# Performance work log

Hardware: AMD Instinct MI355X
Metric: run time of the kernel (lower is better)

Reference implementation:

```python
import jax, jax.numpy as jnp
import numpy as np

B, T, D, H = 4, 2048, 2048, 16
DH = D // H

def setup_inputs() -> dict:
    key = jax.random.key(0)
    ks = jax.random.split(key, 9)
    s = 1.0 / np.sqrt(D)
    return {
        "x": jax.random.normal(ks[0], (B, T, D), dtype=jnp.float32),
        "Wq": jax.random.uniform(ks[1], (D, D), jnp.float32, -s, s),
        "bq": jax.random.uniform(ks[2], (D,), jnp.float32, -s, s),
        "Wk": jax.random.uniform(ks[3], (D, D), jnp.float32, -s, s),
        "bk": jax.random.uniform(ks[4], (D,), jnp.float32, -s, s),
        "Wv": jax.random.uniform(ks[5], (D, D), jnp.float32, -s, s),
        "bv": jax.random.uniform(ks[6], (D,), jnp.float32, -s, s),
        "Wo": jax.random.uniform(ks[7], (D, D), jnp.float32, -s, s),
        "bo": jax.random.uniform(ks[8], (D,), jnp.float32, -s, s),
    }

def reference(x, Wq, bq, Wk, bk, Wv, bv, Wo, bo):
    # projections: [B,T,D] -> [B,H,T,DH]
    def split_heads(y):
        return y.reshape(B, T, H, DH).transpose(0, 2, 1, 3)
    q = split_heads(x @ Wq + bq)
    k = split_heads(x @ Wk + bk)
    v = split_heads(x @ Wv + bv)
    scale = DH ** -0.5
    scores = jnp.einsum('bhtd,bhsd->bhts', q, k) * scale  # [B,H,T,T]
    causal = jnp.tril(jnp.ones((T, T), dtype=bool))
    scores = jnp.where(causal[None, None], scores, -jnp.inf)
    weights = jax.nn.softmax(scores, axis=-1)
    out = jnp.einsum('bhts,bhsd->bhtd', weights, v)  # [B,H,T,DH]
    out = out.transpose(0, 2, 1, 3).reshape(B, T, D)
    return out @ Wo + bo
```

## Files before the change

kernel.cpp:

```cpp
#include <hip/hip_runtime.h>
#include <hip/hip_bf16.h>

#define B_  4
#define T_  2048
#define D_  2048
#define H_  16
#define DH_ 128

typedef __attribute__((ext_vector_type(4))) float f32x4;
typedef __attribute__((ext_vector_type(8))) short short8;
typedef __attribute__((ext_vector_type(4))) _Float16 half4;

__device__ __forceinline__ ushort f2bf(float f) {
    unsigned int u = __builtin_bit_cast(unsigned int, f);
    u += 0x7fffu + ((u >> 16) & 1u);
    return (ushort)(u >> 16);
}
__device__ __forceinline__ ushort f2h(float f) {
    return (ushort)(__builtin_bit_cast(unsigned int, __builtin_amdgcn_cvt_pkrtz(f, f)) & 0xffffu);
}

__device__ __forceinline__ void glds16(const void* g, void* l) {
    __builtin_amdgcn_global_load_lds(
        (const __attribute__((address_space(1))) unsigned int*)g,
        (__attribute__((address_space(3))) unsigned int*)l, 16, 0, 0);
}

__global__ void cast_f32_bf16(const float* __restrict__ x, ushort* __restrict__ xb, int n) {
    int i = (blockIdx.x * 256 + threadIdx.x) * 4;
    if (i < n) {
        float4 v = *(const float4*)(x + i);
        ushort4 o;
        o.x = f2bf(v.x); o.y = f2bf(v.y); o.z = f2bf(v.z); o.w = f2bf(v.w);
        *(ushort4*)(xb + i) = o;
    }
}

__global__ void transpose_cast4(
    const float* __restrict__ W0, const float* __restrict__ W1,
    const float* __restrict__ W2, const float* __restrict__ W3,
    ushort* __restrict__ T0, ushort* __restrict__ T1,
    ushort* __restrict__ T2, ushort* __restrict__ T3)
{
    const int z = blockIdx.z;
    const float* W = (z == 0) ? W0 : (z == 1) ? W1 : (z == 2) ? W2 : W3;
    ushort* Wt     = (z == 0) ? T0 : (z == 1) ? T1 : (z == 2) ? T2 : T3;
    __shared__ float tile[32][33];
    int tx = threadIdx.x, ty = threadIdx.y;
    int n0 = blockIdx.x * 32, k0 = blockIdx.y * 32;
#pragma unroll
    for (int i = 0; i < 4; i++)
        tile[ty + i * 8][tx] = W[(size_t)(k0 + ty + i * 8) * D_ + n0 + tx];
    __syncthreads();
#pragma unroll
    for (int i = 0; i < 4; i++)
        Wt[(size_t)(n0 + ty + i * 8) * D_ + k0 + tx] = f2bf(tile[tx][ty + i * 8]);
}

__global__ __launch_bounds__(256, 3) void gemm_qkv(
    const ushort* __restrict__ A,
    const ushort* __restrict__ Wq, const ushort* __restrict__ Wk, const ushort* __restrict__ Wv,
    const float* __restrict__ bq, const float* __restrict__ bk, const float* __restrict__ bv,
    ushort* __restrict__ Qb, ushort* __restrict__ Kb, ushort* __restrict__ Vtb,
    float qscale, int y0)
{
    extern __shared__ char smem[];
    uint4* sA = (uint4*)smem;
    uint4* sB = (uint4*)(smem + 8192);

    const int tid  = threadIdx.x;
    const int sel  = blockIdx.x >> 4;
    const int row0 = (blockIdx.y + y0) * 128, col0 = (blockIdx.x & 15) * 128;
    const ushort* Bt = (sel == 0) ? Wq : (sel == 1) ? Wk : Wv;
    const float* bias = (sel == 0) ? bq : (sel == 1) ? bk : bv;
    const float oscale = (sel == 0) ? qscale : 1.0f;
    const int K = D_, N = D_;

    const int mA = tid >> 2, g = tid & 3;
    const int gc = g ^ ((mA >> 2) & 3);
    const ushort* pa0 = A  + (size_t)(row0 + mA) * K + gc * 8;
    const ushort* pb0 = Bt + (size_t)(col0 + mA) * K + gc * 8;

    const int lane = tid & 63, w = tid >> 6;
    const int l15 = lane & 15, quad = lane >> 4;
    const int wm = w & 1, wn = w >> 1;
    const int csel = quad ^ ((l15 >> 2) & 3);
    int aoff[4], boff[4];
#pragma unroll
    for (int mt = 0; mt < 4; mt++) aoff[mt] = (wm * 64 + mt * 16 + l15) * 4 + csel;
#pragma unroll
    for (int nt = 0; nt < 4; nt++) boff[nt] = (wn * 64 + nt * 16 + l15) * 4 + csel;

    f32x4 acc[4][4] = {};

    const int kIter = K >> 5;
    for (int kt = 0; kt < kIter; ++kt) {
        if (kt) __syncthreads();
        glds16(pa0 + kt * 32,                     sA + tid);
        glds16(pa0 + kt * 32 + (size_t)64 * K,    sA + tid + 256);
        glds16(pb0 + kt * 32,                     sB + tid);
        glds16(pb0 + kt * 32 + (size_t)64 * K,    sB + tid + 256);
        __syncthreads();
        short8 af[4], bfr[4];
#pragma unroll
        for (int mt = 0; mt < 4; mt++) af[mt]  = __builtin_bit_cast(short8, sA[aoff[mt]]);
#pragma unroll
        for (int nt = 0; nt < 4; nt++) bfr[nt] = __builtin_bit_cast(short8, sB[boff[nt]]);
#pragma unroll
        for (int mt = 0; mt < 4; mt++)
#pragma unroll
            for (int nt = 0; nt < 4; nt++)
                acc[mt][nt] = __builtin_amdgcn_mfma_f32_16x16x32_bf16(af[mt], bfr[nt], acc[mt][nt], 0, 0, 0);
    }

    if (sel < 2) {
        ushort* Cout = (sel == 0) ? Qb : Kb;
#pragma unroll
        for (int nt = 0; nt < 4; nt++) {
            int col = col0 + wn * 64 + nt * 16 + l15;
            float bb = bias[col];
#pragma unroll
            for (int mt = 0; mt < 4; mt++) {
                int rowb = row0 + wm * 64 + mt * 16 + quad * 4;
#pragma unroll
                for (int r = 0; r < 4; ++r)
                    Cout[(size_t)(rowb + r) * N + col] = f2bf((acc[mt][nt][r] + bb) * oscale);
            }
        }
    } else {
        __syncthreads();
        ushort* tr = (ushort*)smem;
#pragma unroll
        for (int nt = 0; nt < 4; nt++) {
            int cl = wn * 64 + nt * 16 + l15;
            float bb = bias[col0 + cl];
#pragma unroll
            for (int mt = 0; mt < 4; mt++) {
                int rl = wm * 64 + mt * 16 + quad * 4;
#pragma unroll
                for (int r = 0; r < 4; ++r)
                    tr[cl * 136 + rl + r] = f2h(acc[mt][nt][r] + bb);
            }
        }
        __syncthreads();
        int b = row0 >> 11, t0 = row0 & (T_ - 1), h = col0 >> 7;
        for (int idx = tid; idx < 2048; idx += 256) {
            int dh = idx >> 4, c = idx & 15;
            uint4 v = *(const uint4*)(tr + dh * 136 + c * 8);
            *(uint4*)(Vtb + (size_t)((b * H_ + h) * DH_ + dh) * T_ + t0 + c * 8) = v;
        }
    }
}

__global__ __launch_bounds__(256, 4) void gemm_bt_f32(
    const ushort* __restrict__ A, const ushort* __restrict__ Bt,
    const float* __restrict__ bias, float* __restrict__ Cout,
    int M, int N, int K)
{
    extern __shared__ char smem[];
    uint4* sA = (uint4*)smem;
    uint4* sB = (uint4*)(smem + 8192);

    const int tid  = threadIdx.x;
    const int row0 = blockIdx.y * 128, col0 = blockIdx.x * 128;

    const int mA = tid >> 2, g = tid & 3;
    const int gc = g ^ ((mA >> 2) & 3);
    const ushort* pa0 = A  + (size_t)(row0 + mA) * K + gc * 8;
    const ushort* pb0 = Bt + (size_t)(col0 + mA) * K + gc * 8;

    const int lane = tid & 63, w = tid >> 6;
    const int l15 = lane & 15, quad = lane >> 4;
    const int wm = w & 1, wn = w >> 1;
    const int csel = quad ^ ((l15 >> 2) & 3);
    int aoff[4], boff[4];
#pragma unroll
    for (int mt = 0; mt < 4; mt++) aoff[mt] = (wm * 64 + mt * 16 + l15) * 4 + csel;
#pragma unroll
    for (int nt = 0; nt < 4; nt++) boff[nt] = (wn * 64 + nt * 16 + l15) * 4 + csel;

    f32x4 acc[4][4] = {};

    const int kIter = K >> 5;
    for (int kt = 0; kt < kIter; ++kt) {
        if (kt) __syncthreads();
        glds16(pa0 + kt * 32,                     sA + tid);
        glds16(pa0 + kt * 32 + (size_t)64 * K,    sA + tid + 256);
        glds16(pb0 + kt * 32,                     sB + tid);
        glds16(pb0 + kt * 32 + (size_t)64 * K,    sB + tid + 256);
        __syncthreads();
        short8 af[4], bfr[4];
#pragma unroll
        for (int mt = 0; mt < 4; mt++) af[mt]  = __builtin_bit_cast(short8, sA[aoff[mt]]);
#pragma unroll
        for (int nt = 0; nt < 4; nt++) bfr[nt] = __builtin_bit_cast(short8, sB[boff[nt]]);
#pragma unroll
        for (int mt = 0; mt < 4; mt++)
#pragma unroll
            for (int nt = 0; nt < 4; nt++)
                acc[mt][nt] = __builtin_amdgcn_mfma_f32_16x16x32_bf16(af[mt], bfr[nt], acc[mt][nt], 0, 0, 0);
    }

#pragma unroll
    for (int nt = 0; nt < 4; nt++) {
        int col = col0 + wn * 64 + nt * 16 + l15;
        float bb = bias[col];
#pragma unroll
        for (int mt = 0; mt < 4; mt++) {
            int rowb = row0 + wm * 64 + mt * 16 + quad * 4;
#pragma unroll
            for (int r = 0; r < 4; ++r)
                Cout[(size_t)(rowb + r) * N + col] = acc[mt][nt][r] + bb;
        }
    }
}

__global__ __launch_bounds__(256, 5) void attn_kernel(
    const ushort* __restrict__ Q, const ushort* __restrict__ K,
    const ushort* __restrict__ Vt, ushort* __restrict__ O)
{
    __shared__ __align__(16) char smem[32768];
    uint4*  kS = (uint4*)smem;
    ushort* vS = (ushort*)(smem + 16384);

    const int tid = threadIdx.x;
    const int bid = blockIdx.x;
    const int slot = bid >> 3;
    const int g = (bid & 7) + 8 * (slot >> 4);
    const int qx = slot & 15;
    const int b = g >> 4, h = g & 15;

    const int lane = tid & 63, w = tid >> 6, l15 = lane & 15, quad = lane >> 4;

    const int krow = tid >> 4;
    const int kchunk = (tid & 15) ^ (krow & 7);
    const ushort* kg = K + ((size_t)(b * T_) + krow) * D_ + h * DH_ + kchunk * 8;

    const int vrow = tid >> 3, vc = tid & 7;
    const ushort* vg = Vt + ((size_t)((b * H_ + h) * DH_) + vrow) * T_ + vc * 8;
    const int vs0 = ((2 * vc    ) ^ (vrow & 15)) * 4;
    const int vs1 = ((2 * vc + 1) ^ (vrow & 15)) * 4;

    const int qts[2] = { qx, 31 - qx };

    for (int e = 0; e < 2; ++e) {
        const int qt = qts[e], q0 = qt * 64;
        const int qbase = q0 + w * 16;

        short8 aq[4];
        {
            const ushort* qp = Q + ((size_t)(b * T_) + qbase + l15) * D_ + h * DH_ + quad * 8;
#pragma unroll
            for (int ks = 0; ks < 4; ++ks)
                aq[ks] = __builtin_bit_cast(short8, *(const uint4*)(qp + ks * 32));
        }

        f32x4 accO[8] = {};
        float mrow = -INFINITY, lrow = 0.f;

        auto tile = [&](int s0, int stMax, bool diag) {
            __syncthreads();
            const ushort* kp = kg + (size_t)s0 * D_;
#pragma unroll
            for (int j = 0; j < 4; ++j) glds16(kp + (size_t)j * 16 * D_, kS + j * 256 + tid);
            const ushort* vp = vg + s0;
            uint4 vv[4];
#pragma unroll
            for (int j = 0; j < 4; ++j) vv[j] = *(const uint4*)(vp + (size_t)j * 32 * T_);
#pragma unroll
            for (int j = 0; j < 4; ++j) {
                ushort* dst = vS + (j * 32 + vrow) * 64;
                *(uint2*)(dst + vs0) = make_uint2(vv[j].x, vv[j].y);
                *(uint2*)(dst + vs1) = make_uint2(vv[j].z, vv[j].w);
            }
            __syncthreads();

            f32x4 sT[4] = {};
#pragma unroll
            for (int ks = 0; ks < 4; ++ks)
#pragma unroll
                for (int st = 0; st < 4; ++st)
                    if (st < stMax) {
                        int row = st * 16 + l15;
                        short8 ak = __builtin_bit_cast(short8, kS[row * 16 + ((ks * 4 + quad) ^ (row & 7))]);
                        sT[st] = __builtin_amdgcn_mfma_f32_16x16x32_bf16(ak, aq[ks], sT[st], 0, 0, 0);
                    }

            if (diag) {
                const int q = qbase + l15;
                const int st = stMax - 1;
#pragma unroll
                for (int r = 0; r < 4; ++r)
                    if (s0 + st * 16 + quad * 4 + r > q) sT[st][r] = -INFINITY;
            }

            float rmax = -INFINITY;
#pragma unroll
            for (int st = 0; st < 4; ++st)
                if (st < stMax)
#pragma unroll
                    for (int r = 0; r < 4; ++r) rmax = fmaxf(rmax, sT[st][r]);
            rmax = fmaxf(rmax, __shfl_xor(rmax, 16));
            rmax = fmaxf(rmax, __shfl_xor(rmax, 32));
            float mnew  = fmaxf(mrow, rmax);
            float alpha = __builtin_amdgcn_exp2f(mrow - mnew);
            mrow = mnew;

            float psum = 0.f;
            half4 pb[4];
#pragma unroll
            for (int st = 0; st < 4; ++st)
                if (st < stMax) {
                    float p0 = __builtin_amdgcn_exp2f(sT[st][0] - mnew);
                    float p1 = __builtin_amdgcn_exp2f(sT[st][1] - mnew);
                    float p2 = __builtin_amdgcn_exp2f(sT[st][2] - mnew);
                    float p3 = __builtin_amdgcn_exp2f(sT[st][3] - mnew);
                    psum += (p0 + p1) + (p2 + p3);
                    uint2 u;
                    u.x = __builtin_bit_cast(unsigned int, __builtin_amdgcn_cvt_pkrtz(p0, p1));
                    u.y = __builtin_bit_cast(unsigned int, __builtin_amdgcn_cvt_pkrtz(p2, p3));
                    pb[st] = __builtin_bit_cast(half4, u);
                }
            psum += __shfl_xor(psum, 16);
            psum += __shfl_xor(psum, 32);
            lrow = lrow * alpha + psum;
#pragma unroll
            for (int nt = 0; nt < 8; ++nt)
#pragma unroll
                for (int r = 0; r < 4; ++r) accO[nt][r] *= alpha;

#pragma unroll
            for (int st = 0; st < 4; ++st)
                if (st < stMax) {
#pragma unroll
                    for (int nt = 0; nt < 8; ++nt) {
                        int dh = nt * 16 + l15;
                        half4 vf = *(const half4*)(vS + dh * 64 + (((st * 4 + quad) ^ l15) * 4));
                        accO[nt] = __builtin_amdgcn_mfma_f32_16x16x16f16(vf, pb[st], accO[nt], 0, 0, 0);
                    }
                }
        };

        for (int it = 0; it < qt; ++it) tile(it * 64, 4, false);
        tile(qt * 64, w + 1, true);

        __syncthreads();
        ushort* eT = (ushort*)smem + w * 2176;
        float inv = 1.0f / lrow;
#pragma unroll
        for (int nt = 0; nt < 8; ++nt) {
            int dh = nt * 16 + quad * 4;
#pragma unroll
            for (int r = 0; r < 4; ++r)
                eT[l15 * 136 + dh + r] = f2bf(accO[nt][r] * inv);
        }
        for (int idx = lane; idx < 256; idx += 64) {
            int row = idx >> 4, c = idx & 15;
            uint4 v = *(const uint4*)(eT + row * 136 + c * 8);
            *(uint4*)(O + ((size_t)(b * T_) + q0 + w * 16 + row) * D_ + h * DH_ + c * 8) = v;
        }
    }
}

extern "C" void kernel_launch(void* const* d_in, const int* in_sizes, int n_in,
                              void* d_out, int out_size, void* d_ws, size_t ws_size,
                              hipStream_t stream) {
    const float* x  = (const float*)d_in[0];
    const float* Wq = (const float*)d_in[1];
    const float* bq = (const float*)d_in[2];
    const float* Wk = (const float*)d_in[3];
    const float* bk = (const float*)d_in[4];
    const float* Wv = (const float*)d_in[5];
    const float* bv = (const float*)d_in[6];
    const float* Wo = (const float*)d_in[7];
    const float* bo = (const float*)d_in[8];

    char* ws = (char*)d_ws;
    const size_t MB = 1u << 20;
    ushort* xb  = (ushort*)(ws);
    ushort* Wqt = (ushort*)(ws + 32 * MB);
    ushort* Wkt = (ushort*)(ws + 40 * MB);
    ushort* Wvt = (ushort*)(ws + 48 * MB);
    ushort* Wot = (ushort*)(ws + 56 * MB);
    ushort* Qb  = (ushort*)(ws + 64 * MB);
    ushort* Kb  = (ushort*)(ws + 96 * MB);
    ushort* Vtb = (ushort*)(ws + 128 * MB);
    ushort* Ob  = (ushort*)(ws + 160 * MB);

    const int M = B_ * T_;
    const float qscale = (float)(0.08838834764831845 * 1.4426950408889634);

    cast_f32_bf16<<<(M * D_) / 1024, 256, 0, stream>>>(x, xb, M * D_);
    dim3 tb(32, 8), tg(D_ / 32, D_ / 32, 4);
    transpose_cast4<<<tg, tb, 0, stream>>>(Wq, Wk, Wv, Wo, Wqt, Wkt, Wvt, Wot);

    gemm_qkv<<<dim3(48, 32), 256, 34816, stream>>>(
        xb, Wqt, Wkt, Wvt, bq, bk, bv, Qb, Kb, Vtb, qscale, 0);
    gemm_qkv<<<dim3(48, 32), 256, 34816, stream>>>(
        xb, Wqt, Wkt, Wvt, bq, bk, bv, Qb, Kb, Vtb, qscale, 32);

    attn_kernel<<<dim3(1024), 256, 0, stream>>>(Qb, Kb, Vtb, Ob);

    gemm_bt_f32<<<dim3(D_ / 128, M / 128), 256, 16384, stream>>>(
        Ob, Wot, bo, (float*)d_out, M, D_, D_);
}
```

Baseline: 628.9 us.

## Merge prep kernels, single QKV GEMM launch, one-tile-per-block attention schedule

Folds the x cast into the weight transpose kernel as an extra grid z-slice and issues the QKV GEMM as one launch instead of two halves. The attention kernel drops the paired light/heavy query-tile scheme and launches 2048 blocks, one query tile each, ordered heaviest-first so the hardware scheduler balances the causal workload. This removes launch overhead and the serial second tile per block, but depends on dynamic dispatch for load balance instead of static pairing.

After: 607.4 us. 1.04x faster.

```diff
diff --git a/kernel.cpp b/kernel.cpp
--- a/kernel.cpp
+++ b/kernel.cpp
@@ -26,27 +26,31 @@
         (__attribute__((address_space(3))) unsigned int*)l, 16, 0, 0);
 }
 
-__global__ void cast_f32_bf16(const float* __restrict__ x, ushort* __restrict__ xb, int n) {
-    int i = (blockIdx.x * 256 + threadIdx.x) * 4;
-    if (i < n) {
-        float4 v = *(const float4*)(x + i);
-        ushort4 o;
-        o.x = f2bf(v.x); o.y = f2bf(v.y); o.z = f2bf(v.z); o.w = f2bf(v.w);
-        *(ushort4*)(xb + i) = o;
-    }
-}
-
-__global__ void transpose_cast4(
+__global__ void prep_kernel(
+    const float* __restrict__ x, ushort* __restrict__ xb,
     const float* __restrict__ W0, const float* __restrict__ W1,
     const float* __restrict__ W2, const float* __restrict__ W3,
     ushort* __restrict__ T0, ushort* __restrict__ T1,
     ushort* __restrict__ T2, ushort* __restrict__ T3)
 {
+    __shared__ float tile[32][33];
     const int z = blockIdx.z;
+    int tx = threadIdx.x, ty = threadIdx.y;
+    if (z == 4) {
+        int blk = blockIdx.y * 64 + blockIdx.x;
+        int tid = ty * 32 + tx;
+        size_t base = (size_t)blk * 4096 + tid * 4;
+#pragma unroll
+        for (int k2 = 0; k2 < 4; ++k2) {
+            float4 v = *(const float4*)(x + base + k2 * 1024);
+            ushort4 o;
+            o.x = f2bf(v.x); o.y = f2bf(v.y); o.z = f2bf(v.z); o.w = f2bf(v.w);
+            *(ushort4*)(xb + base + k2 * 1024) = o;
+        }
+        return;
+    }
     const float* W = (z == 0) ? W0 : (z == 1) ? W1 : (z == 2) ? W2 : W3;
     ushort* Wt     = (z == 0) ? T0 : (z == 1) ? T1 : (z == 2) ? T2 : T3;
-    __shared__ float tile[32][33];
-    int tx = threadIdx.x, ty = threadIdx.y;
     int n0 = blockIdx.x * 32, k0 = blockIdx.y * 32;
 #pragma unroll
     for (int i = 0; i < 4; i++)
@@ -62,7 +66,7 @@
     const ushort* __restrict__ Wq, const ushort* __restrict__ Wk, const ushort* __restrict__ Wv,
     const float* __restrict__ bq, const float* __restrict__ bk, const float* __restrict__ bv,
     ushort* __restrict__ Qb, ushort* __restrict__ Kb, ushort* __restrict__ Vtb,
-    float qscale, int y0)
+    float qscale)
 {
     extern __shared__ char smem[];
     uint4* sA = (uint4*)smem;
@@ -70,7 +74,7 @@
 
     const int tid  = threadIdx.x;
     const int sel  = blockIdx.x >> 4;
-    const int row0 = (blockIdx.y + y0) * 128, col0 = (blockIdx.x & 15) * 128;
+    const int row0 = blockIdx.y * 128, col0 = (blockIdx.x & 15) * 128;
     const ushort* Bt = (sel == 0) ? Wq : (sel == 1) ? Wk : Wv;
     const float* bias = (sel == 0) ? bq : (sel == 1) ? bk : bv;
     const float oscale = (sel == 0) ? qscale : 1.0f;
@@ -225,9 +229,9 @@
 
     const int tid = threadIdx.x;
     const int bid = blockIdx.x;
-    const int slot = bid >> 3;
-    const int g = (bid & 7) + 8 * (slot >> 4);
-    const int qx = slot & 15;
+    const int r  = bid >> 3;
+    const int g  = (bid & 7) + 8 * (r & 7);
+    const int qt = 31 - (r >> 3);
     const int b = g >> 4, h = g & 15;
 
     const int lane = tid & 63, w = tid >> 6, l15 = lane & 15, quad = lane >> 4;
@@ -241,124 +245,120 @@
     const int vs0 = ((2 * vc    ) ^ (vrow & 15)) * 4;
     const int vs1 = ((2 * vc + 1) ^ (vrow & 15)) * 4;
 
-    const int qts[2] = { qx, 31 - qx };
-
-    for (int e = 0; e < 2; ++e) {
-        const int qt = qts[e], q0 = qt * 64;
-        const int qbase = q0 + w * 16;
-
-        short8 aq[4];
-        {
-            const ushort* qp = Q + ((size_t)(b * T_) + qbase + l15) * D_ + h * DH_ + quad * 8;
-#pragma unroll
-            for (int ks = 0; ks < 4; ++ks)
-                aq[ks] = __builtin_bit_cast(short8, *(const uint4*)(qp + ks * 32));
-        }
-
-        f32x4 accO[8] = {};
-        float mrow = -INFINITY, lrow = 0.f;
-
-        auto tile = [&](int s0, int stMax, bool diag) {
-            __syncthreads();
-            const ushort* kp = kg + (size_t)s0 * D_;
-#pragma unroll
-            for (int j = 0; j < 4; ++j) glds16(kp + (size_t)j * 16 * D_, kS + j * 256 + tid);
-            const ushort* vp = vg + s0;
-            uint4 vv[4];
-#pragma unroll
-            for (int j = 0; j < 4; ++j) vv[j] = *(const uint4*)(vp + (size_t)j * 32 * T_);
-#pragma unroll
-            for (int j = 0; j < 4; ++j) {
-                ushort* dst = vS + (j * 32 + vrow) * 64;
-                *(uint2*)(dst + vs0) = make_uint2(vv[j].x, vv[j].y);
-                *(uint2*)(dst + vs1) = make_uint2(vv[j].z, vv[j].w);
-            }
-            __syncthreads();
-
-            f32x4 sT[4] = {};
-#pragma unroll
-            for (int ks = 0; ks < 4; ++ks)
-#pragma unroll
-                for (int st = 0; st < 4; ++st)
-                    if (st < stMax) {
-                        int row = st * 16 + l15;
-                        short8 ak = __builtin_bit_cast(short8, kS[row * 16 + ((ks * 4 + quad) ^ (row & 7))]);
-                        sT[st] = __builtin_amdgcn_mfma_f32_16x16x32_bf16(ak, aq[ks], sT[st], 0, 0, 0);
-                    }
-
-            if (diag) {
-                const int q = qbase + l15;
-                const int st = stMax - 1;
-#pragma unroll
-                for (int r = 0; r < 4; ++r)
-                    if (s0 + st * 16 + quad * 4 + r > q) sT[st][r] = -INFINITY;
-            }
-
-            float rmax = -INFINITY;
-#pragma unroll
-            for (int st = 0; st < 4; ++st)
-                if (st < stMax)
-#pragma unroll
-                    for (int r = 0; r < 4; ++r) rmax = fmaxf(rmax, sT[st][r]);
-            rmax = fmaxf(rmax, __shfl_xor(rmax, 16));
-            rmax = fmaxf(rmax, __shfl_xor(rmax, 32));
-            float mnew  = fmaxf(mrow, rmax);
-            float alpha = __builtin_amdgcn_exp2f(mrow - mnew);
-            mrow = mnew;
-
-            float psum = 0.f;
-            half4 pb[4];
+    const int q0 = qt * 64;
+    const int qbase = q0 + w * 16;
+
+    short8 aq[4];
+    {
+        const ushort* qp = Q + ((size_t)(b * T_) + qbase + l15) * D_ + h * DH_ + quad * 8;
+#pragma unroll
+        for (int ks = 0; ks < 4; ++ks)
+            aq[ks] = __builtin_bit_cast(short8, *(const uint4*)(qp + ks * 32));
+    }
+
+    f32x4 accO[8] = {};
+    float mrow = -INFINITY, lrow = 0.f;
+
+    auto tile = [&](int s0, int stMax, bool diag) {
+        __syncthreads();
+        const ushort* kp = kg + (size_t)s0 * D_;
+#pragma unroll
+        for (int j = 0; j < 4; ++j) glds16(kp + (size_t)j * 16 * D_, kS + j * 256 + tid);
+        const ushort* vp = vg + s0;
+        uint4 vv[4];
+#pragma unroll
+        for (int j = 0; j < 4; ++j) vv[j] = *(const uint4*)(vp + (size_t)j * 32 * T_);
+#pragma unroll
+        for (int j = 0; j < 4; ++j) {
+            ushort* dst = vS + (j * 32 + vrow) * 64;
+            *(uint2*)(dst + vs0) = make_uint2(vv[j].x, vv[j].y);
+            *(uint2*)(dst + vs1) = make_uint2(vv[j].z, vv[j].w);
+        }
+        __syncthreads();
+
+        f32x4 sT[4] = {};
+#pragma unroll
+        for (int ks = 0; ks < 4; ++ks)
 #pragma unroll
             for (int st = 0; st < 4; ++st)
                 if (st < stMax) {
-                    float p0 = __builtin_amdgcn_exp2f(sT[st][0] - mnew);
-                    float p1 = __builtin_amdgcn_exp2f(sT[st][1] - mnew);
-                    float p2 = __builtin_amdgcn_exp2f(sT[st][2] - mnew);
-                    float p3 = __builtin_amdgcn_exp2f(sT[st][3] - mnew);
-                    psum += (p0 + p1) + (p2 + p3);
-                    uint2 u;
-                    u.x = __builtin_bit_cast(unsigned int, __builtin_amdgcn_cvt_pkrtz(p0, p1));
-                    u.y = __builtin_bit_cast(unsigned int, __builtin_amdgcn_cvt_pkrtz(p2, p3));
-                    pb[st] = __builtin_bit_cast(half4, u);
+                    int row = st * 16 + l15;
+                    short8 ak = __builtin_bit_cast(short8, kS[row * 16 + ((ks * 4 + quad) ^ (row & 7))]);
+                    sT[st] = __builtin_amdgcn_mfma_f32_16x16x32_bf16(ak, aq[ks], sT[st], 0, 0, 0);
                 }
-            psum += __shfl_xor(psum, 16);
-            psum += __shfl_xor(psum, 32);
-            lrow = lrow * alpha + psum;
-#pragma unroll
-            for (int nt = 0; nt < 8; ++nt)
-#pragma unroll
-                for (int r = 0; r < 4; ++r) accO[nt][r] *= alpha;
-
-#pragma unroll
-            for (int st = 0; st < 4; ++st)
-                if (st < stMax) {
-#pragma unroll
-                    for (int nt = 0; nt < 8; ++nt) {
-                        int dh = nt * 16 + l15;
-                        half4 vf = *(const half4*)(vS + dh * 64 + (((st * 4 + quad) ^ l15) * 4));
-                        accO[nt] = __builtin_amdgcn_mfma_f32_16x16x16f16(vf, pb[st], accO[nt], 0, 0, 0);
-                    }
+
+        if (diag) {
+            const int q = qbase + l15;
+            const int st = stMax - 1;
+#pragma unroll
+            for (int r2 = 0; r2 < 4; ++r2)
+                if (s0 + st * 16 + quad * 4 + r2 > q) sT[st][r2] = -INFINITY;
+        }
+
+        float rmax = -INFINITY;
+#pragma unroll
+        for (int st = 0; st < 4; ++st)
+            if (st < stMax)
+#pragma unroll
+                for (int r2 = 0; r2 < 4; ++r2) rmax = fmaxf(rmax, sT[st][r2]);
+        rmax = fmaxf(rmax, __shfl_xor(rmax, 16));
+        rmax = fmaxf(rmax, __shfl_xor(rmax, 32));
+        float mnew  = fmaxf(mrow, rmax);
+        float alpha = __builtin_amdgcn_exp2f(mrow - mnew);
+        mrow = mnew;
+
+        float psum = 0.f;
+        half4 pb[4];
+#pragma unroll
+        for (int st = 0; st < 4; ++st)
+            if (st < stMax) {
+                float p0 = __builtin_amdgcn_exp2f(sT[st][0] - mnew);
+                float p1 = __builtin_amdgcn_exp2f(sT[st][1] - mnew);
+                float p2 = __builtin_amdgcn_exp2f(sT[st][2] - mnew);
+                float p3 = __builtin_amdgcn_exp2f(sT[st][3] - mnew);
+                psum += (p0 + p1) + (p2 + p3);
+                uint2 u;
+                u.x = __builtin_bit_cast(unsigned int, __builtin_amdgcn_cvt_pkrtz(p0, p1));
+                u.y = __builtin_bit_cast(unsigned int, __builtin_amdgcn_cvt_pkrtz(p2, p3));
+                pb[st] = __builtin_bit_cast(half4, u);
+            }
+        psum += __shfl_xor(psum, 16);
+        psum += __shfl_xor(psum, 32);
+        lrow = lrow * alpha + psum;
+#pragma unroll
+        for (int nt = 0; nt < 8; ++nt)
+#pragma unroll
+            for (int r2 = 0; r2 < 4; ++r2) accO[nt][r2] *= alpha;
+
+#pragma unroll
+        for (int st = 0; st < 4; ++st)
+            if (st < stMax) {
+#pragma unroll
+                for (int nt = 0; nt < 8; ++nt) {
+                    int dh = nt * 16 + l15;
+                    half4 vf = *(const half4*)(vS + dh * 64 + (((st * 4 + quad) ^ l15) * 4));
+                    accO[nt] = __builtin_amdgcn_mfma_f32_16x16x16f16(vf, pb[st], accO[nt], 0, 0, 0);
                 }
-        };
-
-        for (int it = 0; it < qt; ++it) tile(it * 64, 4, false);
-        tile(qt * 64, w + 1, true);
-
-        __syncthreads();
-        ushort* eT = (ushort*)smem + w * 2176;
-        float inv = 1.0f / lrow;
-#pragma unroll
-        for (int nt = 0; nt < 8; ++nt) {
-            int dh = nt * 16 + quad * 4;
-#pragma unroll
-            for (int r = 0; r < 4; ++r)
-                eT[l15 * 136 + dh + r] = f2bf(accO[nt][r] * inv);
-        }
-        for (int idx = lane; idx < 256; idx += 64) {
-            int row = idx >> 4, c = idx & 15;
-            uint4 v = *(const uint4*)(eT + row * 136 + c * 8);
-            *(uint4*)(O + ((size_t)(b * T_) + q0 + w * 16 + row) * D_ + h * DH_ + c * 8) = v;
-        }
+            }
+    };
+
+    for (int it = 0; it < qt; ++it) tile(it * 64, 4, false);
+    tile(qt * 64, w + 1, true);
+
+    __syncthreads();
+    ushort* eT = (ushort*)smem + w * 2176;
+    float inv = 1.0f / lrow;
+#pragma unroll
+    for (int nt = 0; nt < 8; ++nt) {
+        int dh = nt * 16 + quad * 4;
+#pragma unroll
+        for (int r2 = 0; r2 < 4; ++r2)
+            eT[l15 * 136 + dh + r2] = f2bf(accO[nt][r2] * inv);
+    }
+    for (int idx = lane; idx < 256; idx += 64) {
+        int row = idx >> 4, c = idx & 15;
+        uint4 v = *(const uint4*)(eT + row * 136 + c * 8);
+        *(uint4*)(O + ((size_t)(b * T_) + q0 + w * 16 + row) * D_ + h * DH_ + c * 8) = v;
     }
 }
 
@@ -390,16 +390,13 @@
     const int M = B_ * T_;
     const float qscale = (float)(0.08838834764831845 * 1.4426950408889634);
 
-    cast_f32_bf16<<<(M * D_) / 1024, 256, 0, stream>>>(x, xb, M * D_);
-    dim3 tb(32, 8), tg(D_ / 32, D_ / 32, 4);
-    transpose_cast4<<<tg, tb, 0, stream>>>(Wq, Wk, Wv, Wo, Wqt, Wkt, Wvt, Wot);
-
-    gemm_qkv<<<dim3(48, 32), 256, 34816, stream>>>(
-        xb, Wqt, Wkt, Wvt, bq, bk, bv, Qb, Kb, Vtb, qscale, 0);
-    gemm_qkv<<<dim3(48, 32), 256, 34816, stream>>>(
-        xb, Wqt, Wkt, Wvt, bq, bk, bv, Qb, Kb, Vtb, qscale, 32);
-
-    attn_kernel<<<dim3(1024), 256, 0, stream>>>(Qb, Kb, Vtb, Ob);
+    dim3 tb(32, 8), tg(D_ / 32, D_ / 32, 5);
+    prep_kernel<<<tg, tb, 0, stream>>>(x, xb, Wq, Wk, Wv, Wo, Wqt, Wkt, Wvt, Wot);
+
+    gemm_qkv<<<dim3(48, M / 128), 256, 34816, stream>>>(
+        xb, Wqt, Wkt, Wvt, bq, bk, bv, Qb, Kb, Vtb, qscale);
+
+    attn_kernel<<<dim3(2048), 256, 0, stream>>>(Qb, Kb, Vtb, Ob);
 
     gemm_bt_f32<<<dim3(D_ / 128, M / 128), 256, 16384, stream>>>(
         Ob, Wot, bo, (float*)d_out, M, D_, D_);
```
